# Kernel tuning notes

Hardware: AMD Instinct MI355X
Metric: run time of the kernel (lower is better)

The kernel has to match this reference:

```python
import jax, jax.numpy as jnp
import numpy as np

B, S, D = 16, 2048, 128
NEG = -1000000000.0


def setup_inputs() -> dict:
    key = jax.random.key(0)
    kq, kk, kv = jax.random.split(key, 3)
    q = jax.random.normal(kq, (B, S, D), dtype=jnp.float32)
    k = jax.random.normal(kk, (B, S, D), dtype=jnp.float32)
    v = jax.random.normal(kv, (B, S, D), dtype=jnp.float32)
    # causal mask: True entries are masked out (filled with -1e9)
    mask = jnp.broadcast_to(
        jnp.triu(jnp.ones((S, S), dtype=bool), k=1)[None, :, :], (B, S, S)
    )
    return {"q": q, "k": k, "v": v, "mask": mask}


def reference(q, k, v, mask):
    # attn = q @ k^T / sqrt(d_k), masked_fill, softmax over keys, attn @ v
    scale = jnp.sqrt(jnp.asarray(D, dtype=q.dtype))
    attn = jnp.einsum("bqd,bkd->bqk", q, k) / scale
    attn = jnp.where(mask, jnp.asarray(NEG, dtype=attn.dtype), attn)
    attn = jax.nn.softmax(attn, axis=2)
    out = jnp.einsum("bqk,bkd->bqd", attn, v)
    return (out, attn)
```

## Files before the change

kernel.cpp:

```cpp
#include <hip/hip_runtime.h>

#define B_ 16
#define S_ 2048
#define D_ 128

typedef __attribute__((ext_vector_type(8))) short bf16x8;
typedef __attribute__((ext_vector_type(4))) float f32x4;
typedef __attribute__((ext_vector_type(2))) unsigned int u32x2;
typedef __attribute__((ext_vector_type(4))) unsigned int u32x4;

__device__ __forceinline__ unsigned short f2bf(float f) {
    unsigned int u = __builtin_bit_cast(unsigned int, f);
    u += 0x7fff + ((u >> 16) & 1);
    return (unsigned short)(u >> 16);
}

__device__ __forceinline__ void gload16(const void* g, void* l) {
    __builtin_amdgcn_global_load_lds(
        (const __attribute__((address_space(1))) void*)g,
        (__attribute__((address_space(3))) void*)l, 16, 0, 0);
}

#define WAITV(n) asm volatile("s_waitcnt vmcnt(" #n ")" ::: "memory")

__global__ __launch_bounds__(256, 4)
void conv_k(const float* __restrict__ kg, char* __restrict__ kws)
{
    const int bid = blockIdx.x;
    const float* src = kg + ((long)bid << 13);
    char* dst = kws + ((long)bid << 14);
#pragma unroll
    for (int it = 0; it < 4; ++it) {
        const int c = threadIdx.x + it * 256;
        const int r = c >> 4, j = c & 15;
        f32x4 a = *(const f32x4*)(src + r * 128 + j * 8);
        f32x4 cc = *(const f32x4*)(src + r * 128 + j * 8 + 4);
        u32x4 p;
        p[0] = (unsigned)f2bf(a[0]) | ((unsigned)f2bf(a[1]) << 16);
        p[1] = (unsigned)f2bf(a[2]) | ((unsigned)f2bf(a[3]) << 16);
        p[2] = (unsigned)f2bf(cc[0]) | ((unsigned)f2bf(cc[1]) << 16);
        p[3] = (unsigned)f2bf(cc[2]) | ((unsigned)f2bf(cc[3]) << 16);
        *(u32x4*)(dst + r * 256 + ((j ^ (r & 7)) << 4)) = p;
    }
}

__global__ __launch_bounds__(256, 2)
void conv_v(const float* __restrict__ vg, char* __restrict__ vws)
{
    __shared__ float lt[64 * 132];
    const int bid = blockIdx.x;
    const float* src = vg + ((long)bid << 13);
    char* dst = vws + ((long)bid << 14);
#pragma unroll
    for (int it = 0; it < 8; ++it) {
        const int c = threadIdx.x + it * 256;
        const int r = c >> 5, q = c & 31;
        *(f32x4*)(lt + r * 132 + q * 4) = *(const f32x4*)(src + r * 128 + q * 4);
    }
    __syncthreads();
#pragma unroll
    for (int it = 0; it < 4; ++it) {
        const int c = threadIdx.x + it * 256;
        const int d = c >> 3, jc = c & 7;
        unsigned short e[8];
#pragma unroll
        for (int ee = 0; ee < 8; ++ee) e[ee] = f2bf(lt[(jc * 8 + ee) * 132 + d]);
        u32x4 p;
        p[0] = (unsigned)e[0] | ((unsigned)e[1] << 16);
        p[1] = (unsigned)e[2] | ((unsigned)e[3] << 16);
        p[2] = (unsigned)e[4] | ((unsigned)e[5] << 16);
        p[3] = (unsigned)e[6] | ((unsigned)e[7] << 16);
        *(u32x4*)(dst + d * 128 + ((jc ^ (d & 7)) << 4)) = p;
    }
}

__device__ __forceinline__ int qtile_of(int b, int t) {
    const int f = (t & 1) ? (t >> 1) : (31 - (t >> 1));
    return (b & 8) ? (31 - f) : f;
}

__global__ __launch_bounds__(256, 2)
void flash_fwd(const float* __restrict__ qg, const char* __restrict__ kws,
               const char* __restrict__ vws, float* __restrict__ outg,
               float* __restrict__ lg)
{
    __shared__ char kT[2][16384];
    __shared__ char vT[2][16384];
    __shared__ unsigned short pT[4][16 * 64];

    const int tid = threadIdx.x, lane = tid & 63, w = tid >> 6;
    const int l15 = lane & 15, l4 = lane >> 4;
    const int bid = blockIdx.x;
    const int b = bid >> 5;
    const int qt = qtile_of(b, bid & 31);
    const int q0 = qt * 64;
    const float scale = 0.088388347648318447f;

    bf16x8 qf[4];
    {
        const float* qrow = qg + ((long)b * S_ + q0 + w * 16 + l15) * D_;
#pragma unroll
        for (int kk = 0; kk < 4; ++kk) {
            const int d0 = kk * 32 + l4 * 8;
            f32x4 a = *(const f32x4*)(qrow + d0);
            f32x4 c = *(const f32x4*)(qrow + d0 + 4);
            bf16x8 tt;
            tt[0] = (short)f2bf(a[0]); tt[1] = (short)f2bf(a[1]);
            tt[2] = (short)f2bf(a[2]); tt[3] = (short)f2bf(a[3]);
            tt[4] = (short)f2bf(c[0]); tt[5] = (short)f2bf(c[1]);
            tt[6] = (short)f2bf(c[2]); tt[7] = (short)f2bf(c[3]);
            qf[kk] = tt;
        }
    }
    WAITV(0);

    float sum[4] = {0.f, 0.f, 0.f, 0.f};
    f32x4 oacc[8];
#pragma unroll
    for (int n = 0; n < 8; ++n) oacc[n] = (f32x4){0.f, 0.f, 0.f, 0.f};

    const char* kb0 = kws + ((long)(b * 32) << 14);
    const char* vb0 = vws + ((long)(b * 32) << 14);

#pragma unroll
    for (int it = 0; it < 4; ++it)
        gload16(kb0 + (w * 4 + it) * 1024 + lane * 16, &kT[0][(w * 4 + it) * 1024]);
#pragma unroll
    for (int it = 0; it < 4; ++it)
        gload16(vb0 + (w * 4 + it) * 1024 + lane * 16, &vT[0][(w * 4 + it) * 1024]);

    int buf = 0;
    for (int kt = 0; kt <= qt; ++kt) {
        if (kt < qt) {
            const char* kn = kb0 + ((long)(kt + 1) << 14);
            const char* vn = vb0 + ((long)(kt + 1) << 14);
#pragma unroll
            for (int it = 0; it < 4; ++it)
                gload16(kn + (w * 4 + it) * 1024 + lane * 16, &kT[buf ^ 1][(w * 4 + it) * 1024]);
#pragma unroll
            for (int it = 0; it < 4; ++it)
                gload16(vn + (w * 4 + it) * 1024 + lane * 16, &vT[buf ^ 1][(w * 4 + it) * 1024]);
            WAITV(8);
        } else {
            WAITV(0);
        }
        __builtin_amdgcn_s_barrier();
        __builtin_amdgcn_sched_barrier(0);

        f32x4 acc[4];
#pragma unroll
        for (int n = 0; n < 4; ++n) {
            f32x4 a = {0.f, 0.f, 0.f, 0.f};
            const int krow = n * 16 + l15;
            const int rb = krow * 256;
            const int swz = (krow & 7) << 4;
#pragma unroll
            for (int kk = 0; kk < 4; ++kk) {
                bf16x8 bf = *(const bf16x8*)(&kT[buf][rb + ((l4 * 16 + kk * 64) ^ swz)]);
                a = __builtin_amdgcn_mfma_f32_16x16x32_bf16(qf[kk], bf, a, 0, 0, 0);
            }
            acc[n] = a;
        }

        const bool diag = (kt == qt);
#pragma unroll
        for (int n = 0; n < 4; ++n)
#pragma unroll
            for (int r = 0; r < 4; ++r) {
                float p;
                if (diag && (n * 16 + l15 > w * 16 + l4 * 4 + r)) p = 0.f;
                else p = __expf(acc[n][r] * scale);
                sum[r] += p;
                const int prow = l4 * 4 + r;
                *(unsigned short*)((char*)&pT[w][0] + prow * 128 +
                                   ((n * 32 + l15 * 2) ^ ((prow & 7) << 4))) = f2bf(p);
            }
        asm volatile("s_waitcnt lgkmcnt(0)" ::: "memory");
        __builtin_amdgcn_sched_barrier(0);

        bf16x8 pa[2];
#pragma unroll
        for (int kk = 0; kk < 2; ++kk)
            pa[kk] = *(const bf16x8*)((const char*)&pT[w][0] + l15 * 128 +
                                      ((l4 * 16 + kk * 64) ^ ((l15 & 7) << 4)));
#pragma unroll
        for (int n = 0; n < 8; ++n) {
            const int vrow = n * 16 + l15;
            const int rb2 = vrow * 128;
            const int swz2 = (vrow & 7) << 4;
#pragma unroll
            for (int kk = 0; kk < 2; ++kk) {
                bf16x8 bv = *(const bf16x8*)(&vT[buf][rb2 + ((l4 * 16 + kk * 64) ^ swz2)]);
                oacc[n] = __builtin_amdgcn_mfma_f32_16x16x32_bf16(pa[kk], bv, oacc[n], 0, 0, 0);
            }
        }
        __builtin_amdgcn_sched_barrier(0);
        __builtin_amdgcn_s_barrier();
        buf ^= 1;
    }

#pragma unroll
    for (int off = 1; off < 16; off <<= 1)
#pragma unroll
        for (int r = 0; r < 4; ++r)
            sum[r] += __shfl_xor(sum[r], off, 64);
    float invl[4];
#pragma unroll
    for (int r = 0; r < 4; ++r) invl[r] = 1.f / sum[r];

    float* obase = outg + ((long)b * S_ + q0 + w * 16) * D_;
#pragma unroll
    for (int n = 0; n < 8; ++n)
#pragma unroll
        for (int r = 0; r < 4; ++r)
            obase[(long)(l4 * 4 + r) * D_ + n * 16 + l15] = oacc[n][r] * invl[r];
    if (l15 == 0) {
#pragma unroll
        for (int r = 0; r < 4; ++r)
            lg[(long)b * S_ + q0 + w * 16 + l4 * 4 + r] = invl[r];
    }
}

__global__ __launch_bounds__(256, 2)
void attn_write(const float* __restrict__ qg, const char* __restrict__ kws,
                const float* __restrict__ lg, float* __restrict__ attng)
{
    __shared__ char kT[2][16384];

    const int tid = threadIdx.x, lane = tid & 63, w = tid >> 6;
    const int l15 = lane & 15, l4 = lane >> 4;
    const int bid = blockIdx.x;
    const int b = bid >> 5;
    const int qt = qtile_of(b, bid & 31);
    const int q0 = qt * 64;
    const float scale = 0.088388347648318447f;

    bf16x8 qf[4];
    {
        const float* qrow = qg + ((long)b * S_ + q0 + w * 16 + l15) * D_;
#pragma unroll
        for (int kk = 0; kk < 4; ++kk) {
            const int d0 = kk * 32 + l4 * 8;
            f32x4 a = *(const f32x4*)(qrow + d0);
            f32x4 c = *(const f32x4*)(qrow + d0 + 4);
            bf16x8 tt;
            tt[0] = (short)f2bf(a[0]); tt[1] = (short)f2bf(a[1]);
            tt[2] = (short)f2bf(a[2]); tt[3] = (short)f2bf(a[3]);
            tt[4] = (short)f2bf(c[0]); tt[5] = (short)f2bf(c[1]);
            tt[6] = (short)f2bf(c[2]); tt[7] = (short)f2bf(c[3]);
            qf[kk] = tt;
        }
    }
    float invl[4];
#pragma unroll
    for (int r = 0; r < 4; ++r)
        invl[r] = lg[(long)b * S_ + q0 + w * 16 + l4 * 4 + r];
    WAITV(0);

    const char* kb0 = kws + ((long)(b * 32) << 14);
    float* attn_base = attng + ((long)b * S_ + q0) * S_;

#pragma unroll
    for (int it = 0; it < 4; ++it)
        gload16(kb0 + (w * 4 + it) * 1024 + lane * 16, &kT[0][(w * 4 + it) * 1024]);

    int buf = 0;
    for (int kt = 0; kt <= qt; ++kt) {
        if (kt < qt) {
            const char* kn = kb0 + ((long)(kt + 1) << 14);
#pragma unroll
            for (int it = 0; it < 4; ++it)
                gload16(kn + (w * 4 + it) * 1024 + lane * 16, &kT[buf ^ 1][(w * 4 + it) * 1024]);
            if (kt == 0) { WAITV(4); } else { WAITV(20); }
        } else {
            if (kt == 0) { WAITV(0); } else { WAITV(16); }
        }
        __builtin_amdgcn_s_barrier();
        __builtin_amdgcn_sched_barrier(0);

        f32x4 acc[4];
#pragma unroll
        for (int n = 0; n < 4; ++n) {
            f32x4 a = {0.f, 0.f, 0.f, 0.f};
            const int krow = n * 16 + l15;
            const int rb = krow * 256;
            const int swz = (krow & 7) << 4;
#pragma unroll
            for (int kk = 0; kk < 4; ++kk) {
                bf16x8 bf = *(const bf16x8*)(&kT[buf][rb + ((l4 * 16 + kk * 64) ^ swz)]);
                a = __builtin_amdgcn_mfma_f32_16x16x32_bf16(qf[kk], bf, a, 0, 0, 0);
            }
            acc[n] = a;
        }

        const bool diag = (kt == qt);
        float* abase = attn_base + (long)(w * 16) * S_ + kt * 64;
#pragma unroll
        for (int n = 0; n < 4; ++n)
#pragma unroll
            for (int r = 0; r < 4; ++r) {
                float p;
                if (diag && (n * 16 + l15 > w * 16 + l4 * 4 + r)) p = 0.f;
                else p = __expf(acc[n][r] * scale) * invl[r];
                abase[(long)(l4 * 4 + r) * S_ + n * 16 + l15] = p;
            }
        __builtin_amdgcn_sched_barrier(0);
        __builtin_amdgcn_s_barrier();
        buf ^= 1;
    }

    const int col0 = (qt + 1) * 64;
    if (col0 < S_) {
        const int nch = (S_ - col0) >> 2;
        const f32x4 z = {0.f, 0.f, 0.f, 0.f};
        for (int row = w; row < 64; row += 4) {
            float* rbase = attn_base + (long)row * S_ + col0;
            for (int c = lane; c < nch; c += 64)
                *(f32x4*)(rbase + c * 4) = z;
        }
    }
}

__global__ __launch_bounds__(256, 2)
void attn_fallback(const float* __restrict__ qg, const float* __restrict__ kg,
                   const float* __restrict__ vg,
                   float* __restrict__ outg, float* __restrict__ attng)
{
    __shared__ unsigned short kT[64 * 128];
    __shared__ unsigned short vT[128 * 64];
    __shared__ unsigned short pT[4][16 * 64];
    const int tid = threadIdx.x, lane = tid & 63, w = tid >> 6;
    const int l15 = lane & 15, l4 = lane >> 4;
    const int bid = blockIdx.x;
    const int b = bid >> 5, qt = 31 - (bid & 31), q0 = qt * 64;
    const float scale = 0.088388347648318447f;
    bf16x8 qf[4];
    {
        const float* qrow = qg + ((long)b * S_ + q0 + w * 16 + l15) * D_;
#pragma unroll
        for (int kk = 0; kk < 4; ++kk) {
            const int d0 = kk * 32 + l4 * 8;
            f32x4 a = *(const f32x4*)(qrow + d0);
            f32x4 c = *(const f32x4*)(qrow + d0 + 4);
            bf16x8 t;
            t[0] = (short)f2bf(a[0]); t[1] = (short)f2bf(a[1]);
            t[2] = (short)f2bf(a[2]); t[3] = (short)f2bf(a[3]);
            t[4] = (short)f2bf(c[0]); t[5] = (short)f2bf(c[1]);
            t[6] = (short)f2bf(c[2]); t[7] = (short)f2bf(c[3]);
            qf[kk] = t;
        }
    }
    float m[4], l[4];
#pragma unroll
    for (int r = 0; r < 4; ++r) { m[r] = -1e30f; l[r] = 0.f; }
    for (int kt = 0; kt <= qt; ++kt) {
        __syncthreads();
        {
            const float* kbase = kg + ((long)b * S_ + kt * 64) * D_;
#pragma unroll
            for (int it = 0; it < 8; ++it) {
                const int c = tid + it * 256, row = c >> 5, dc = c & 31;
                f32x4 a = *(const f32x4*)(kbase + row * D_ + dc * 4);
                u32x2 p;
                p[0] = (unsigned)f2bf(a[0]) | ((unsigned)f2bf(a[1]) << 16);
                p[1] = (unsigned)f2bf(a[2]) | ((unsigned)f2bf(a[3]) << 16);
                *(u32x2*)((char*)kT + row * 256 + ((dc * 8) ^ ((row & 7) << 4))) = p;
            }
        }
        __syncthreads();
        f32x4 acc[4];
#pragma unroll
        for (int n = 0; n < 4; ++n) {
            f32x4 a = {0.f, 0.f, 0.f, 0.f};
            const int krow = n * 16 + l15, rb = krow * 256, swz = (krow & 7) << 4;
#pragma unroll
            for (int kk = 0; kk < 4; ++kk) {
                bf16x8 bf = *(const bf16x8*)((const char*)kT + rb + ((l4 * 16 + kk * 64) ^ swz));
                a = __builtin_amdgcn_mfma_f32_16x16x32_bf16(qf[kk], bf, a, 0, 0, 0);
            }
            acc[n] = a;
        }
        const bool diag = (kt == qt);
        float tm[4] = {-3e38f, -3e38f, -3e38f, -3e38f};
#pragma unroll
        for (int n = 0; n < 4; ++n)
#pragma unroll
            for (int r = 0; r < 4; ++r) {
                float s = acc[n][r] * scale;
                if (diag && (n * 16 + l15 > w * 16 + l4 * 4 + r)) s = -3e38f;
                acc[n][r] = s; tm[r] = fmaxf(tm[r], s);
            }
#pragma unroll
        for (int off = 1; off < 16; off <<= 1)
#pragma unroll
            for (int r = 0; r < 4; ++r) tm[r] = fmaxf(tm[r], __shfl_xor(tm[r], off, 64));
        float sum[4], mn[4];
#pragma unroll
        for (int r = 0; r < 4; ++r) {
            mn[r] = fmaxf(m[r], tm[r]);
            float s0 = 0.f;
#pragma unroll
            for (int n = 0; n < 4; ++n) s0 += __expf(acc[n][r] - mn[r]);
            sum[r] = s0;
        }
#pragma unroll
        for (int off = 1; off < 16; off <<= 1)
#pragma unroll
            for (int r = 0; r < 4; ++r) sum[r] += __shfl_xor(sum[r], off, 64);
#pragma unroll
        for (int r = 0; r < 4; ++r) { l[r] = l[r] * __expf(m[r] - mn[r]) + sum[r]; m[r] = mn[r]; }
    }
    float invl[4];
#pragma unroll
    for (int r = 0; r < 4; ++r) invl[r] = 1.f / l[r];
    f32x4 oacc[8];
#pragma unroll
    for (int n = 0; n < 8; ++n) oacc[n] = (f32x4){0.f, 0.f, 0.f, 0.f};
    float* attn_base = attng + ((long)b * S_ + q0) * S_;
    for (int kt = 0; kt <= qt; ++kt) {
        __syncthreads();
        {
            const float* kbase = kg + ((long)b * S_ + kt * 64) * D_;
#pragma unroll
            for (int it = 0; it < 8; ++it) {
                const int c = tid + it * 256, row = c >> 5, dc = c & 31;
                f32x4 a = *(const f32x4*)(kbase + row * D_ + dc * 4);
                u32x2 p;
                p[0] = (unsigned)f2bf(a[0]) | ((unsigned)f2bf(a[1]) << 16);
                p[1] = (unsigned)f2bf(a[2]) | ((unsigned)f2bf(a[3]) << 16);
                *(u32x2*)((char*)kT + row * 256 + ((dc * 8) ^ ((row & 7) << 4))) = p;
            }
        }
        {
            const float* vbase = vg + ((long)b * S_ + kt * 64) * D_;
#pragma unroll
            for (int it = 0; it < 8; ++it) {
                const int c = tid + it * 256, kr = c & 63, dq = c >> 6;
                f32x4 a = *(const f32x4*)(vbase + kr * D_ + dq * 4);
#pragma unroll
                for (int j = 0; j < 4; ++j) {
                    const int d = dq * 4 + j;
                    *(unsigned short*)((char*)vT + d * 128 + ((kr * 2) ^ ((d & 7) << 4))) = f2bf(a[j]);
                }
            }
        }
        __syncthreads();
        f32x4 acc[4];
#pragma unroll
        for (int n = 0; n < 4; ++n) {
            f32x4 a = {0.f, 0.f, 0.f, 0.f};
            const int krow = n * 16 + l15, rb = krow * 256, swz = (krow & 7) << 4;
#pragma unroll
            for (int kk = 0; kk < 4; ++kk) {
                bf16x8 bf = *(const bf16x8*)((const char*)kT + rb + ((l4 * 16 + kk * 64) ^ swz));
                a = __builtin_amdgcn_mfma_f32_16x16x32_bf16(qf[kk], bf, a, 0, 0, 0);
            }
            acc[n] = a;
        }
        const bool diag = (kt == qt);
#pragma unroll
        for (int n = 0; n < 4; ++n)
#pragma unroll
            for (int r = 0; r < 4; ++r) {
                float s = acc[n][r] * scale;
                if (diag && (n * 16 + l15 > w * 16 + l4 * 4 + r)) s = -3e38f;
                const float p = __expf(s - m[r]) * invl[r];
                attn_base[(long)(w * 16 + l4 * 4 + r) * S_ + kt * 64 + n * 16 + l15] = p;
                const int prow = l4 * 4 + r;
                *(unsigned short*)((char*)&pT[w][0] + prow * 128 + ((n * 32 + l15 * 2) ^ ((prow & 7) << 4))) = f2bf(p);
            }
        asm volatile("s_waitcnt lgkmcnt(0)" ::: "memory");
        __builtin_amdgcn_sched_barrier(0);
        bf16x8 pa[2];
#pragma unroll
        for (int kk = 0; kk < 2; ++kk)
            pa[kk] = *(const bf16x8*)((const char*)&pT[w][0] + l15 * 128 + ((l4 * 16 + kk * 64) ^ ((l15 & 7) << 4)));
#pragma unroll
        for (int n = 0; n < 8; ++n) {
            const int vrow = n * 16 + l15, rb = vrow * 128, swz = (vrow & 7) << 4;
#pragma unroll
            for (int kk = 0; kk < 2; ++kk) {
                bf16x8 bv = *(const bf16x8*)((const char*)vT + rb + ((l4 * 16 + kk * 64) ^ swz));
                oacc[n] = __builtin_amdgcn_mfma_f32_16x16x32_bf16(pa[kk], bv, oacc[n], 0, 0, 0);
            }
        }
    }
    {
        float* obase = outg + ((long)b * S_ + q0 + w * 16) * D_;
#pragma unroll
        for (int n = 0; n < 8; ++n)
#pragma unroll
            for (int r = 0; r < 4; ++r)
                obase[(long)(l4 * 4 + r) * D_ + n * 16 + l15] = oacc[n][r];
    }
    {
        const int col0 = (qt + 1) * 64;
        if (col0 < S_) {
            const int nch = (S_ - col0) >> 2;
            const f32x4 z = {0.f, 0.f, 0.f, 0.f};
            for (int row = w; row < 64; row += 4) {
                float* rbase = attn_base + (long)row * S_ + col0;
                for (int c = lane; c < nch; c += 64)
                    *(f32x4*)(rbase + c * 4) = z;
            }
        }
    }
}

extern "C" void kernel_launch(void* const* d_in, const int* in_sizes, int n_in,
                              void* d_out, int out_size, void* d_ws, size_t ws_size,
                              hipStream_t stream) {
    const float* q = (const float*)d_in[0];
    const float* k = (const float*)d_in[1];
    const float* v = (const float*)d_in[2];
    float* out  = (float*)d_out;
    float* attn = out + (long)B_ * S_ * D_;
    const size_t NEED = 131072 + 2u * 8388608u;
    if (ws_size >= NEED) {
        float* lg = (float*)d_ws;
        char* kws = (char*)d_ws + 131072;
        char* vws = kws + 8388608;
        conv_k<<<dim3(512), dim3(256), 0, stream>>>(k, kws);
        conv_v<<<dim3(512), dim3(256), 0, stream>>>(v, vws);
        flash_fwd<<<dim3(512), dim3(256), 0, stream>>>(q, kws, vws, out, lg);
        attn_write<<<dim3(512), dim3(256), 0, stream>>>(q, kws, lg, attn);
    } else {
        attn_fallback<<<dim3(512), dim3(256), 0, stream>>>(q, k, v, out, attn);
    }
}
```

Measured before the change: 135.2 us.

## Merge K/V conversion kernels and split attn_write key range across two blocks

Fuses the K and V bf16 conversion kernels into one 1024-block launch to remove a kernel launch and its tail. attn_write now uses 1024 blocks, with each query tile's key tiles split in half between two blocks and the zero-fill of the upper triangle split by row halves. Occupancy is raised to 4 blocks per CU. This targets the tail imbalance and low parallelism of writing the large attention matrix, at the cost of loading Q and invl twice per tile and pipelining over shorter loops. conv_kv keeps the V path's 33KB LDS buffer but is now declared with 4 blocks per SM, which may limit occupancy for the K blocks.

```diff
diff --git a/kernel.cpp b/kernel.cpp
--- a/kernel.cpp
+++ b/kernel.cpp
@@ -24,53 +24,52 @@
 #define WAITV(n) asm volatile("s_waitcnt vmcnt(" #n ")" ::: "memory")
 
 __global__ __launch_bounds__(256, 4)
-void conv_k(const float* __restrict__ kg, char* __restrict__ kws)
-{
-    const int bid = blockIdx.x;
-    const float* src = kg + ((long)bid << 13);
-    char* dst = kws + ((long)bid << 14);
-#pragma unroll
-    for (int it = 0; it < 4; ++it) {
-        const int c = threadIdx.x + it * 256;
-        const int r = c >> 4, j = c & 15;
-        f32x4 a = *(const f32x4*)(src + r * 128 + j * 8);
-        f32x4 cc = *(const f32x4*)(src + r * 128 + j * 8 + 4);
-        u32x4 p;
-        p[0] = (unsigned)f2bf(a[0]) | ((unsigned)f2bf(a[1]) << 16);
-        p[1] = (unsigned)f2bf(a[2]) | ((unsigned)f2bf(a[3]) << 16);
-        p[2] = (unsigned)f2bf(cc[0]) | ((unsigned)f2bf(cc[1]) << 16);
-        p[3] = (unsigned)f2bf(cc[2]) | ((unsigned)f2bf(cc[3]) << 16);
-        *(u32x4*)(dst + r * 256 + ((j ^ (r & 7)) << 4)) = p;
-    }
-}
-
-__global__ __launch_bounds__(256, 2)
-void conv_v(const float* __restrict__ vg, char* __restrict__ vws)
+void conv_kv(const float* __restrict__ kg, const float* __restrict__ vg,
+             char* __restrict__ kws, char* __restrict__ vws)
 {
     __shared__ float lt[64 * 132];
     const int bid = blockIdx.x;
-    const float* src = vg + ((long)bid << 13);
-    char* dst = vws + ((long)bid << 14);
-#pragma unroll
-    for (int it = 0; it < 8; ++it) {
-        const int c = threadIdx.x + it * 256;
-        const int r = c >> 5, q = c & 31;
-        *(f32x4*)(lt + r * 132 + q * 4) = *(const f32x4*)(src + r * 128 + q * 4);
-    }
-    __syncthreads();
-#pragma unroll
-    for (int it = 0; it < 4; ++it) {
-        const int c = threadIdx.x + it * 256;
-        const int d = c >> 3, jc = c & 7;
-        unsigned short e[8];
-#pragma unroll
-        for (int ee = 0; ee < 8; ++ee) e[ee] = f2bf(lt[(jc * 8 + ee) * 132 + d]);
-        u32x4 p;
-        p[0] = (unsigned)e[0] | ((unsigned)e[1] << 16);
-        p[1] = (unsigned)e[2] | ((unsigned)e[3] << 16);
-        p[2] = (unsigned)e[4] | ((unsigned)e[5] << 16);
-        p[3] = (unsigned)e[6] | ((unsigned)e[7] << 16);
-        *(u32x4*)(dst + d * 128 + ((jc ^ (d & 7)) << 4)) = p;
+    if (bid < 512) {
+        const float* src = kg + ((long)bid << 13);
+        char* dst = kws + ((long)bid << 14);
+#pragma unroll
+        for (int it = 0; it < 4; ++it) {
+            const int c = threadIdx.x + it * 256;
+            const int r = c >> 4, j = c & 15;
+            f32x4 a = *(const f32x4*)(src + r * 128 + j * 8);
+            f32x4 cc = *(const f32x4*)(src + r * 128 + j * 8 + 4);
+            u32x4 p;
+            p[0] = (unsigned)f2bf(a[0]) | ((unsigned)f2bf(a[1]) << 16);
+            p[1] = (unsigned)f2bf(a[2]) | ((unsigned)f2bf(a[3]) << 16);
+            p[2] = (unsigned)f2bf(cc[0]) | ((unsigned)f2bf(cc[1]) << 16);
+            p[3] = (unsigned)f2bf(cc[2]) | ((unsigned)f2bf(cc[3]) << 16);
+            *(u32x4*)(dst + r * 256 + ((j ^ (r & 7)) << 4)) = p;
+        }
+    } else {
+        const int vb = bid - 512;
+        const float* src = vg + ((long)vb << 13);
+        char* dst = vws + ((long)vb << 14);
+#pragma unroll
+        for (int it = 0; it < 8; ++it) {
+            const int c = threadIdx.x + it * 256;
+            const int r = c >> 5, q = c & 31;
+            *(f32x4*)(lt + r * 132 + q * 4) = *(const f32x4*)(src + r * 128 + q * 4);
+        }
+        __syncthreads();
+#pragma unroll
+        for (int it = 0; it < 4; ++it) {
+            const int c = threadIdx.x + it * 256;
+            const int d = c >> 3, jc = c & 7;
+            unsigned short e[8];
+#pragma unroll
+            for (int ee = 0; ee < 8; ++ee) e[ee] = f2bf(lt[(jc * 8 + ee) * 132 + d]);
+            u32x4 p;
+            p[0] = (unsigned)e[0] | ((unsigned)e[1] << 16);
+            p[1] = (unsigned)e[2] | ((unsigned)e[3] << 16);
+            p[2] = (unsigned)e[4] | ((unsigned)e[5] << 16);
+            p[3] = (unsigned)e[6] | ((unsigned)e[7] << 16);
+            *(u32x4*)(dst + d * 128 + ((jc ^ (d & 7)) << 4)) = p;
+        }
     }
 }
 
@@ -221,7 +220,7 @@
     }
 }
 
-__global__ __launch_bounds__(256, 2)
+__global__ __launch_bounds__(256, 4)
 void attn_write(const float* __restrict__ qg, const char* __restrict__ kws,
                 const float* __restrict__ lg, float* __restrict__ attng)
 {
@@ -230,9 +229,14 @@
     const int tid = threadIdx.x, lane = tid & 63, w = tid >> 6;
     const int l15 = lane & 15, l4 = lane >> 4;
     const int bid = blockIdx.x;
-    const int b = bid >> 5;
-    const int qt = qtile_of(b, bid & 31);
+    const int b  = bid >> 6;
+    const int t2 = bid & 63;
+    const int qt = qtile_of(b, t2 >> 1);
+    const int h  = t2 & 1;
     const int q0 = qt * 64;
+    const int nt = qt + 1;
+    const int k0 = h ? (nt >> 1) : 0;
+    const int k1 = h ? nt : (nt >> 1);
     const float scale = 0.088388347648318447f;
 
     bf16x8 qf[4];
@@ -260,60 +264,63 @@
     const char* kb0 = kws + ((long)(b * 32) << 14);
     float* attn_base = attng + ((long)b * S_ + q0) * S_;
 
-#pragma unroll
-    for (int it = 0; it < 4; ++it)
-        gload16(kb0 + (w * 4 + it) * 1024 + lane * 16, &kT[0][(w * 4 + it) * 1024]);
-
-    int buf = 0;
-    for (int kt = 0; kt <= qt; ++kt) {
-        if (kt < qt) {
-            const char* kn = kb0 + ((long)(kt + 1) << 14);
-#pragma unroll
-            for (int it = 0; it < 4; ++it)
-                gload16(kn + (w * 4 + it) * 1024 + lane * 16, &kT[buf ^ 1][(w * 4 + it) * 1024]);
-            if (kt == 0) { WAITV(4); } else { WAITV(20); }
-        } else {
-            if (kt == 0) { WAITV(0); } else { WAITV(16); }
-        }
-        __builtin_amdgcn_s_barrier();
-        __builtin_amdgcn_sched_barrier(0);
-
-        f32x4 acc[4];
-#pragma unroll
-        for (int n = 0; n < 4; ++n) {
-            f32x4 a = {0.f, 0.f, 0.f, 0.f};
-            const int krow = n * 16 + l15;
-            const int rb = krow * 256;
-            const int swz = (krow & 7) << 4;
-#pragma unroll
-            for (int kk = 0; kk < 4; ++kk) {
-                bf16x8 bf = *(const bf16x8*)(&kT[buf][rb + ((l4 * 16 + kk * 64) ^ swz)]);
-                a = __builtin_amdgcn_mfma_f32_16x16x32_bf16(qf[kk], bf, a, 0, 0, 0);
-            }
-            acc[n] = a;
-        }
-
-        const bool diag = (kt == qt);
-        float* abase = attn_base + (long)(w * 16) * S_ + kt * 64;
-#pragma unroll
-        for (int n = 0; n < 4; ++n)
-#pragma unroll
-            for (int r = 0; r < 4; ++r) {
-                float p;
-                if (diag && (n * 16 + l15 > w * 16 + l4 * 4 + r)) p = 0.f;
-                else p = __expf(acc[n][r] * scale) * invl[r];
-                abase[(long)(l4 * 4 + r) * S_ + n * 16 + l15] = p;
-            }
-        __builtin_amdgcn_sched_barrier(0);
-        __builtin_amdgcn_s_barrier();
-        buf ^= 1;
-    }
-
-    const int col0 = (qt + 1) * 64;
+    if (k1 > k0) {
+#pragma unroll
+        for (int it = 0; it < 4; ++it)
+            gload16(kb0 + ((long)k0 << 14) + (w * 4 + it) * 1024 + lane * 16,
+                    &kT[0][(w * 4 + it) * 1024]);
+
+        int buf = 0;
+        for (int kt = k0; kt < k1; ++kt) {
+            const bool pf = (kt + 1 < k1);
+            if (pf) {
+                const char* kn = kb0 + ((long)(kt + 1) << 14);
+#pragma unroll
+                for (int it = 0; it < 4; ++it)
+                    gload16(kn + (w * 4 + it) * 1024 + lane * 16, &kT[buf ^ 1][(w * 4 + it) * 1024]);
+            }
+            if (kt == k0) { if (pf) { WAITV(4); } else { WAITV(0); } }
+            else          { if (pf) { WAITV(20); } else { WAITV(16); } }
+            __builtin_amdgcn_s_barrier();
+            __builtin_amdgcn_sched_barrier(0);
+
+            f32x4 acc[4];
+#pragma unroll
+            for (int n = 0; n < 4; ++n) {
+                f32x4 a = {0.f, 0.f, 0.f, 0.f};
+                const int krow = n * 16 + l15;
+                const int rb = krow * 256;
+                const int swz = (krow & 7) << 4;
+#pragma unroll
+                for (int kk = 0; kk < 4; ++kk) {
+                    bf16x8 bf = *(const bf16x8*)(&kT[buf][rb + ((l4 * 16 + kk * 64) ^ swz)]);
+                    a = __builtin_amdgcn_mfma_f32_16x16x32_bf16(qf[kk], bf, a, 0, 0, 0);
+                }
+                acc[n] = a;
+            }
+
+            const bool diag = (kt == qt);
+            float* abase = attn_base + (long)(w * 16) * S_ + kt * 64;
+#pragma unroll
+            for (int n = 0; n < 4; ++n)
+#pragma unroll
+                for (int r = 0; r < 4; ++r) {
+                    float p;
+                    if (diag && (n * 16 + l15 > w * 16 + l4 * 4 + r)) p = 0.f;
+                    else p = __expf(acc[n][r] * scale) * invl[r];
+                    abase[(long)(l4 * 4 + r) * S_ + n * 16 + l15] = p;
+                }
+            __builtin_amdgcn_sched_barrier(0);
+            __builtin_amdgcn_s_barrier();
+            buf ^= 1;
+        }
+    }
+
+    const int col0 = nt * 64;
     if (col0 < S_) {
         const int nch = (S_ - col0) >> 2;
         const f32x4 z = {0.f, 0.f, 0.f, 0.f};
-        for (int row = w; row < 64; row += 4) {
+        for (int row = h * 32 + w; row < h * 32 + 32; row += 4) {
             float* rbase = attn_base + (long)row * S_ + col0;
             for (int c = lane; c < nch; c += 64)
                 *(f32x4*)(rbase + c * 4) = z;
@@ -520,10 +527,9 @@
         float* lg = (float*)d_ws;
         char* kws = (char*)d_ws + 131072;
         char* vws = kws + 8388608;
-        conv_k<<<dim3(512), dim3(256), 0, stream>>>(k, kws);
-        conv_v<<<dim3(512), dim3(256), 0, stream>>>(v, vws);
+        conv_kv<<<dim3(1024), dim3(256), 0, stream>>>(k, v, kws, vws);
         flash_fwd<<<dim3(512), dim3(256), 0, stream>>>(q, kws, vws, out, lg);
-        attn_write<<<dim3(512), dim3(256), 0, stream>>>(q, kws, lg, attn);
+        attn_write<<<dim3(1024), dim3(256), 0, stream>>>(q, kws, lg, attn);
     } else {
         attn_fallback<<<dim3(512), dim3(256), 0, stream>>>(q, k, v, out, attn);
     }
```

After: 133.0 us. About the same (-1.6%).

## Restructure attention into row-sum pass and fused attn-write plus PV pass

Applied to the files above, without the earlier changes.

Merges the K and V bf16 conversion kernels into one launch. Replaces the flash forward plus attn-write pair with a lightweight sum-of-exp pass (QK^T only, which also zero-fills the masked upper region of attn) and a second pass that writes normalized attention and computes P·V together. This moves the PV matmul and V loads out of the first pass so it can run at higher occupancy, and removes the extra launch. It also adds s_setprio around the MFMA blocks. The cost is that the second pass now holds more LDS and does exp, the global attn store and the MFMAs in the same loop.

```diff
diff --git a/kernel.cpp b/kernel.cpp
--- a/kernel.cpp
+++ b/kernel.cpp
@@ -24,53 +24,52 @@
 #define WAITV(n) asm volatile("s_waitcnt vmcnt(" #n ")" ::: "memory")
 
 __global__ __launch_bounds__(256, 4)
-void conv_k(const float* __restrict__ kg, char* __restrict__ kws)
-{
-    const int bid = blockIdx.x;
-    const float* src = kg + ((long)bid << 13);
-    char* dst = kws + ((long)bid << 14);
-#pragma unroll
-    for (int it = 0; it < 4; ++it) {
-        const int c = threadIdx.x + it * 256;
-        const int r = c >> 4, j = c & 15;
-        f32x4 a = *(const f32x4*)(src + r * 128 + j * 8);
-        f32x4 cc = *(const f32x4*)(src + r * 128 + j * 8 + 4);
-        u32x4 p;
-        p[0] = (unsigned)f2bf(a[0]) | ((unsigned)f2bf(a[1]) << 16);
-        p[1] = (unsigned)f2bf(a[2]) | ((unsigned)f2bf(a[3]) << 16);
-        p[2] = (unsigned)f2bf(cc[0]) | ((unsigned)f2bf(cc[1]) << 16);
-        p[3] = (unsigned)f2bf(cc[2]) | ((unsigned)f2bf(cc[3]) << 16);
-        *(u32x4*)(dst + r * 256 + ((j ^ (r & 7)) << 4)) = p;
-    }
-}
-
-__global__ __launch_bounds__(256, 2)
-void conv_v(const float* __restrict__ vg, char* __restrict__ vws)
+void conv_kv(const float* __restrict__ kg, const float* __restrict__ vg,
+             char* __restrict__ kws, char* __restrict__ vws)
 {
     __shared__ float lt[64 * 132];
     const int bid = blockIdx.x;
-    const float* src = vg + ((long)bid << 13);
-    char* dst = vws + ((long)bid << 14);
-#pragma unroll
-    for (int it = 0; it < 8; ++it) {
-        const int c = threadIdx.x + it * 256;
-        const int r = c >> 5, q = c & 31;
-        *(f32x4*)(lt + r * 132 + q * 4) = *(const f32x4*)(src + r * 128 + q * 4);
-    }
-    __syncthreads();
-#pragma unroll
-    for (int it = 0; it < 4; ++it) {
-        const int c = threadIdx.x + it * 256;
-        const int d = c >> 3, jc = c & 7;
-        unsigned short e[8];
-#pragma unroll
-        for (int ee = 0; ee < 8; ++ee) e[ee] = f2bf(lt[(jc * 8 + ee) * 132 + d]);
-        u32x4 p;
-        p[0] = (unsigned)e[0] | ((unsigned)e[1] << 16);
-        p[1] = (unsigned)e[2] | ((unsigned)e[3] << 16);
-        p[2] = (unsigned)e[4] | ((unsigned)e[5] << 16);
-        p[3] = (unsigned)e[6] | ((unsigned)e[7] << 16);
-        *(u32x4*)(dst + d * 128 + ((jc ^ (d & 7)) << 4)) = p;
+    if (bid < 512) {
+        const float* src = kg + ((long)bid << 13);
+        char* dst = kws + ((long)bid << 14);
+#pragma unroll
+        for (int it = 0; it < 4; ++it) {
+            const int c = threadIdx.x + it * 256;
+            const int r = c >> 4, j = c & 15;
+            f32x4 a = *(const f32x4*)(src + r * 128 + j * 8);
+            f32x4 cc = *(const f32x4*)(src + r * 128 + j * 8 + 4);
+            u32x4 p;
+            p[0] = (unsigned)f2bf(a[0]) | ((unsigned)f2bf(a[1]) << 16);
+            p[1] = (unsigned)f2bf(a[2]) | ((unsigned)f2bf(a[3]) << 16);
+            p[2] = (unsigned)f2bf(cc[0]) | ((unsigned)f2bf(cc[1]) << 16);
+            p[3] = (unsigned)f2bf(cc[2]) | ((unsigned)f2bf(cc[3]) << 16);
+            *(u32x4*)(dst + r * 256 + ((j ^ (r & 7)) << 4)) = p;
+        }
+    } else {
+        const int vb = bid - 512;
+        const float* src = vg + ((long)vb << 13);
+        char* dst = vws + ((long)vb << 14);
+#pragma unroll
+        for (int it = 0; it < 8; ++it) {
+            const int c = threadIdx.x + it * 256;
+            const int r = c >> 5, q = c & 31;
+            *(f32x4*)(lt + r * 132 + q * 4) = *(const f32x4*)(src + r * 128 + q * 4);
+        }
+        __syncthreads();
+#pragma unroll
+        for (int it = 0; it < 4; ++it) {
+            const int c = threadIdx.x + it * 256;
+            const int d = c >> 3, jc = c & 7;
+            unsigned short e[8];
+#pragma unroll
+            for (int ee = 0; ee < 8; ++ee) e[ee] = f2bf(lt[(jc * 8 + ee) * 132 + d]);
+            u32x4 p;
+            p[0] = (unsigned)e[0] | ((unsigned)e[1] << 16);
+            p[1] = (unsigned)e[2] | ((unsigned)e[3] << 16);
+            p[2] = (unsigned)e[4] | ((unsigned)e[5] << 16);
+            p[3] = (unsigned)e[6] | ((unsigned)e[7] << 16);
+            *(u32x4*)(dst + d * 128 + ((jc ^ (d & 7)) << 4)) = p;
+        }
     }
 }
 
@@ -79,14 +78,11 @@
     return (b & 8) ? (31 - f) : f;
 }
 
-__global__ __launch_bounds__(256, 2)
-void flash_fwd(const float* __restrict__ qg, const char* __restrict__ kws,
-               const char* __restrict__ vws, float* __restrict__ outg,
-               float* __restrict__ lg)
+__global__ __launch_bounds__(256, 4)
+void sumexp(const float* __restrict__ qg, const char* __restrict__ kws,
+            float* __restrict__ lg, float* __restrict__ attng)
 {
     __shared__ char kT[2][16384];
-    __shared__ char vT[2][16384];
-    __shared__ unsigned short pT[4][16 * 64];
 
     const int tid = threadIdx.x, lane = tid & 63, w = tid >> 6;
     const int l15 = lane & 15, l4 = lane >> 4;
@@ -115,32 +111,21 @@
     WAITV(0);
 
     float sum[4] = {0.f, 0.f, 0.f, 0.f};
-    f32x4 oacc[8];
-#pragma unroll
-    for (int n = 0; n < 8; ++n) oacc[n] = (f32x4){0.f, 0.f, 0.f, 0.f};
-
     const char* kb0 = kws + ((long)(b * 32) << 14);
-    const char* vb0 = vws + ((long)(b * 32) << 14);
 
 #pragma unroll
     for (int it = 0; it < 4; ++it)
         gload16(kb0 + (w * 4 + it) * 1024 + lane * 16, &kT[0][(w * 4 + it) * 1024]);
-#pragma unroll
-    for (int it = 0; it < 4; ++it)
-        gload16(vb0 + (w * 4 + it) * 1024 + lane * 16, &vT[0][(w * 4 + it) * 1024]);
 
     int buf = 0;
     for (int kt = 0; kt <= qt; ++kt) {
-        if (kt < qt) {
+        const bool pf = (kt < qt);
+        if (pf) {
             const char* kn = kb0 + ((long)(kt + 1) << 14);
-            const char* vn = vb0 + ((long)(kt + 1) << 14);
 #pragma unroll
             for (int it = 0; it < 4; ++it)
                 gload16(kn + (w * 4 + it) * 1024 + lane * 16, &kT[buf ^ 1][(w * 4 + it) * 1024]);
-#pragma unroll
-            for (int it = 0; it < 4; ++it)
-                gload16(vn + (w * 4 + it) * 1024 + lane * 16, &vT[buf ^ 1][(w * 4 + it) * 1024]);
-            WAITV(8);
+            WAITV(4);
         } else {
             WAITV(0);
         }
@@ -148,6 +133,7 @@
         __builtin_amdgcn_sched_barrier(0);
 
         f32x4 acc[4];
+        __builtin_amdgcn_s_setprio(1);
 #pragma unroll
         for (int n = 0; n < 4; ++n) {
             f32x4 a = {0.f, 0.f, 0.f, 0.f};
@@ -161,39 +147,16 @@
             }
             acc[n] = a;
         }
+        __builtin_amdgcn_s_setprio(0);
 
         const bool diag = (kt == qt);
 #pragma unroll
         for (int n = 0; n < 4; ++n)
 #pragma unroll
             for (int r = 0; r < 4; ++r) {
-                float p;
-                if (diag && (n * 16 + l15 > w * 16 + l4 * 4 + r)) p = 0.f;
-                else p = __expf(acc[n][r] * scale);
-                sum[r] += p;
-                const int prow = l4 * 4 + r;
-                *(unsigned short*)((char*)&pT[w][0] + prow * 128 +
-                                   ((n * 32 + l15 * 2) ^ ((prow & 7) << 4))) = f2bf(p);
-            }
-        asm volatile("s_waitcnt lgkmcnt(0)" ::: "memory");
-        __builtin_amdgcn_sched_barrier(0);
-
-        bf16x8 pa[2];
-#pragma unroll
-        for (int kk = 0; kk < 2; ++kk)
-            pa[kk] = *(const bf16x8*)((const char*)&pT[w][0] + l15 * 128 +
-                                      ((l4 * 16 + kk * 64) ^ ((l15 & 7) << 4)));
-#pragma unroll
-        for (int n = 0; n < 8; ++n) {
-            const int vrow = n * 16 + l15;
-            const int rb2 = vrow * 128;
-            const int swz2 = (vrow & 7) << 4;
-#pragma unroll
-            for (int kk = 0; kk < 2; ++kk) {
-                bf16x8 bv = *(const bf16x8*)(&vT[buf][rb2 + ((l4 * 16 + kk * 64) ^ swz2)]);
-                oacc[n] = __builtin_amdgcn_mfma_f32_16x16x32_bf16(pa[kk], bv, oacc[n], 0, 0, 0);
-            }
-        }
+                if (!(diag && (n * 16 + l15 > w * 16 + l4 * 4 + r)))
+                    sum[r] += __expf(acc[n][r] * scale);
+            }
         __builtin_amdgcn_sched_barrier(0);
         __builtin_amdgcn_s_barrier();
         buf ^= 1;
@@ -204,28 +167,33 @@
 #pragma unroll
         for (int r = 0; r < 4; ++r)
             sum[r] += __shfl_xor(sum[r], off, 64);
-    float invl[4];
-#pragma unroll
-    for (int r = 0; r < 4; ++r) invl[r] = 1.f / sum[r];
-
-    float* obase = outg + ((long)b * S_ + q0 + w * 16) * D_;
-#pragma unroll
-    for (int n = 0; n < 8; ++n)
+    if (l15 == 0) {
 #pragma unroll
         for (int r = 0; r < 4; ++r)
-            obase[(long)(l4 * 4 + r) * D_ + n * 16 + l15] = oacc[n][r] * invl[r];
-    if (l15 == 0) {
-#pragma unroll
-        for (int r = 0; r < 4; ++r)
-            lg[(long)b * S_ + q0 + w * 16 + l4 * 4 + r] = invl[r];
+            lg[(long)b * S_ + q0 + w * 16 + l4 * 4 + r] = 1.f / sum[r];
+    }
+
+    float* attn_base = attng + ((long)b * S_ + q0) * S_;
+    const int col0 = (qt + 1) * 64;
+    if (col0 < S_) {
+        const int nch = (S_ - col0) >> 2;
+        const f32x4 z = {0.f, 0.f, 0.f, 0.f};
+        for (int row = w; row < 64; row += 4) {
+            float* rbase = attn_base + (long)row * S_ + col0;
+            for (int c = lane; c < nch; c += 64)
+                *(f32x4*)(rbase + c * 4) = z;
+        }
     }
 }
 
 __global__ __launch_bounds__(256, 2)
-void attn_write(const float* __restrict__ qg, const char* __restrict__ kws,
-                const float* __restrict__ lg, float* __restrict__ attng)
+void attn_pv(const float* __restrict__ qg, const char* __restrict__ kws,
+             const char* __restrict__ vws, const float* __restrict__ lg,
+             float* __restrict__ outg, float* __restrict__ attng)
 {
     __shared__ char kT[2][16384];
+    __shared__ char vT[2][16384];
+    __shared__ unsigned short pT[4][16 * 64];
 
     const int tid = threadIdx.x, lane = tid & 63, w = tid >> 6;
     const int l15 = lane & 15, l4 = lane >> 4;
@@ -257,28 +225,41 @@
         invl[r] = lg[(long)b * S_ + q0 + w * 16 + l4 * 4 + r];
     WAITV(0);
 
+    f32x4 oacc[8];
+#pragma unroll
+    for (int n = 0; n < 8; ++n) oacc[n] = (f32x4){0.f, 0.f, 0.f, 0.f};
+
     const char* kb0 = kws + ((long)(b * 32) << 14);
+    const char* vb0 = vws + ((long)(b * 32) << 14);
     float* attn_base = attng + ((long)b * S_ + q0) * S_;
 
 #pragma unroll
     for (int it = 0; it < 4; ++it)
         gload16(kb0 + (w * 4 + it) * 1024 + lane * 16, &kT[0][(w * 4 + it) * 1024]);
+#pragma unroll
+    for (int it = 0; it < 4; ++it)
+        gload16(vb0 + (w * 4 + it) * 1024 + lane * 16, &vT[0][(w * 4 + it) * 1024]);
 
     int buf = 0;
     for (int kt = 0; kt <= qt; ++kt) {
-        if (kt < qt) {
+        const bool pf = (kt < qt);
+        if (pf) {
             const char* kn = kb0 + ((long)(kt + 1) << 14);
+            const char* vn = vb0 + ((long)(kt + 1) << 14);
 #pragma unroll
             for (int it = 0; it < 4; ++it)
                 gload16(kn + (w * 4 + it) * 1024 + lane * 16, &kT[buf ^ 1][(w * 4 + it) * 1024]);
-            if (kt == 0) { WAITV(4); } else { WAITV(20); }
-        } else {
-            if (kt == 0) { WAITV(0); } else { WAITV(16); }
-        }
+#pragma unroll
+            for (int it = 0; it < 4; ++it)
+                gload16(vn + (w * 4 + it) * 1024 + lane * 16, &vT[buf ^ 1][(w * 4 + it) * 1024]);
+        }
+        if (kt == 0) { if (pf) { WAITV(8); } else { WAITV(0); } }
+        else         { if (pf) { WAITV(24); } else { WAITV(16); } }
         __builtin_amdgcn_s_barrier();
         __builtin_amdgcn_sched_barrier(0);
 
         f32x4 acc[4];
+        __builtin_amdgcn_s_setprio(1);
 #pragma unroll
         for (int n = 0; n < 4; ++n) {
             f32x4 a = {0.f, 0.f, 0.f, 0.f};
@@ -292,6 +273,7 @@
             }
             acc[n] = a;
         }
+        __builtin_amdgcn_s_setprio(0);
 
         const bool diag = (kt == qt);
         float* abase = attn_base + (long)(w * 16) * S_ + kt * 64;
@@ -301,24 +283,44 @@
             for (int r = 0; r < 4; ++r) {
                 float p;
                 if (diag && (n * 16 + l15 > w * 16 + l4 * 4 + r)) p = 0.f;
-                else p = __expf(acc[n][r] * scale) * invl[r];
-                abase[(long)(l4 * 4 + r) * S_ + n * 16 + l15] = p;
-            }
+                else p = __expf(acc[n][r] * scale);
+                abase[(long)(l4 * 4 + r) * S_ + n * 16 + l15] = p * invl[r];
+                const int prow = l4 * 4 + r;
+                *(unsigned short*)((char*)&pT[w][0] + prow * 128 +
+                                   ((n * 32 + l15 * 2) ^ ((prow & 7) << 4))) = f2bf(p);
+            }
+        asm volatile("s_waitcnt lgkmcnt(0)" ::: "memory");
+        __builtin_amdgcn_sched_barrier(0);
+
+        bf16x8 pa[2];
+#pragma unroll
+        for (int kk = 0; kk < 2; ++kk)
+            pa[kk] = *(const bf16x8*)((const char*)&pT[w][0] + l15 * 128 +
+                                      ((l4 * 16 + kk * 64) ^ ((l15 & 7) << 4)));
+        __builtin_amdgcn_s_setprio(1);
+#pragma unroll
+        for (int n = 0; n < 8; ++n) {
+            const int vrow = n * 16 + l15;
+            const int rb2 = vrow * 128;
+            const int swz2 = (vrow & 7) << 4;
+#pragma unroll
+            for (int kk = 0; kk < 2; ++kk) {
+                bf16x8 bv = *(const bf16x8*)(&vT[buf][rb2 + ((l4 * 16 + kk * 64) ^ swz2)]);
+                oacc[n] = __builtin_amdgcn_mfma_f32_16x16x32_bf16(pa[kk], bv, oacc[n], 0, 0, 0);
+            }
+        }
+        __builtin_amdgcn_s_setprio(0);
         __builtin_amdgcn_sched_barrier(0);
         __builtin_amdgcn_s_barrier();
         buf ^= 1;
     }
 
-    const int col0 = (qt + 1) * 64;
-    if (col0 < S_) {
-        const int nch = (S_ - col0) >> 2;
-        const f32x4 z = {0.f, 0.f, 0.f, 0.f};
-        for (int row = w; row < 64; row += 4) {
-            float* rbase = attn_base + (long)row * S_ + col0;
-            for (int c = lane; c < nch; c += 64)
-                *(f32x4*)(rbase + c * 4) = z;
-        }
-    }
+    float* obase = outg + ((long)b * S_ + q0 + w * 16) * D_;
+#pragma unroll
+    for (int n = 0; n < 8; ++n)
+#pragma unroll
+        for (int r = 0; r < 4; ++r)
+            obase[(long)(l4 * 4 + r) * D_ + n * 16 + l15] = oacc[n][r] * invl[r];
 }
 
 __global__ __launch_bounds__(256, 2)
@@ -520,10 +522,9 @@
         float* lg = (float*)d_ws;
         char* kws = (char*)d_ws + 131072;
         char* vws = kws + 8388608;
-        conv_k<<<dim3(512), dim3(256), 0, stream>>>(k, kws);
-        conv_v<<<dim3(512), dim3(256), 0, stream>>>(v, vws);
-        flash_fwd<<<dim3(512), dim3(256), 0, stream>>>(q, kws, vws, out, lg);
-        attn_write<<<dim3(512), dim3(256), 0, stream>>>(q, kws, lg, attn);
+        conv_kv<<<dim3(1024), dim3(256), 0, stream>>>(k, v, kws, vws);
+        sumexp<<<dim3(512), dim3(256), 0, stream>>>(q, kws, lg, attn);
+        attn_pv<<<dim3(512), dim3(256), 0, stream>>>(q, kws, vws, lg, out, attn);
     } else {
         attn_fallback<<<dim3(512), dim3(256), 0, stream>>>(q, k, v, out, attn);
     }
```

New measurement: 126.9 us. 1.07x faster.
